# Optimization experiments

Hardware: AMD Instinct MI355X
Metric: run time of the kernel (lower is better)

Reference implementation:

```python
import jax, jax.numpy as jnp
import numpy as np

B, S, D, H = 8, 1024, 512, 8
HD = D // H
NEG = -1000000000.0
LN_EPS = 1e-5


def setup_inputs() -> dict:
    key = jax.random.key(0)
    ks = jax.random.split(key, 16)
    sc = 0.02
    inp = {
        "query": jax.random.normal(ks[0], (B, S, D), jnp.float32),
        "inputs": jax.random.normal(ks[1], (B, S, D), jnp.float32),
        "ren_mat": jax.random.uniform(ks[2], (B, S, S), jnp.float32) * 5.0,
        "timestamp": jax.random.normal(ks[3], (B, S, S), jnp.float32),
        # causal mask: True where attention is disallowed (strictly upper triangular)
        "mask": jnp.triu(jnp.ones((1, S, S), jnp.bool_), k=1),
        "Wq": jax.random.normal(ks[4], (D, D), jnp.float32) * sc,
        "bq": jnp.zeros((D,), jnp.float32),
        "Wk": jax.random.normal(ks[5], (D, D), jnp.float32) * sc,
        "bk": jnp.zeros((D,), jnp.float32),
        "Wv": jax.random.normal(ks[6], (D, D), jnp.float32) * sc,
        "bv": jnp.zeros((D,), jnp.float32),
        "Wo": jax.random.normal(ks[7], (D, D), jnp.float32) * sc,
        "bo": jnp.zeros((D,), jnp.float32),
        "W1": jax.random.normal(ks[8], (D, D), jnp.float32) * sc,
        "b1": jnp.zeros((D,), jnp.float32),
        "ln_g": jnp.ones((D,), jnp.float32),
        "ln_b": jnp.zeros((D,), jnp.float32),
        "l1": jax.random.uniform(ks[9], (1,), jnp.float32),
    }
    return inp


def reference(query, inputs, ren_mat, timestamp, mask,
              Wq, bq, Wk, bk, Wv, bv, Wo, bo, W1, b1, ln_g, ln_b, l1):
    # QKV projections (qk_same=False path; q,k,v all computed from `inputs`)
    def proj(x, W, b):
        return (x @ W.T + b).reshape(B, S, H, HD).transpose(0, 2, 1, 3)  # (B,H,S,HD)

    q = proj(inputs, Wq, bq)
    k = proj(inputs, Wk, bk)
    v = proj(inputs, Wv, bv)

    m = mask[:, None]  # (1,1,S,S), broadcasts over batch & heads

    scores = jnp.einsum("bhqd,bhkd->bhqk", q, k) / jnp.sqrt(jnp.float32(HD))
    scores = jnp.where(m, NEG, scores)
    prob_attn = jax.nn.softmax(scores, axis=-1)

    # memory blend: log10(ren+1) and exp(-|t|), each masked, summed, softmaxed
    ren_feat = jnp.where(m, NEG, jnp.log10(ren_mat + 1.0)[:, None])      # (B,H,S,S)
    time_stamp = jnp.where(m, NEG, jnp.exp(-jnp.abs(timestamp))[:, None])
    mem_attn = jax.nn.softmax(ren_feat + time_stamp, axis=-1)

    l = l1  # (1,) learned blend coefficient
    prob_attn = (1.0 - l) * prob_attn + l * mem_attn

    out = jnp.einsum("bhqk,bhkd->bhqd", prob_attn, v)
    out = out.transpose(0, 2, 1, 3).reshape(B, S, D)
    out = out @ Wo.T + bo

    # residual FFN + layernorm (dropout disabled / eval mode)
    out = out + (out @ W1.T + b1)
    mu = jnp.mean(out, axis=-1, keepdims=True)
    var = jnp.var(out, axis=-1, keepdims=True)
    out = (out - mu) / jnp.sqrt(var + LN_EPS) * ln_g + ln_b
    return out
```

## Files before the change

kernel.cpp:

```cpp
#include <hip/hip_runtime.h>
#include <math.h>

constexpr int kB = 8, kS = 1024, kD = 512, kH = 8, kHD = 64;
constexpr int kM = kB * kS;

typedef __attribute__((ext_vector_type(8))) short s8v;
typedef __attribute__((ext_vector_type(4))) float f4v;
typedef __attribute__((ext_vector_type(4))) unsigned short u4v;

__device__ __forceinline__ unsigned short f2bf(float f) {
    union { float f; unsigned int u; } c; c.f = f;
    unsigned int u = c.u + 0x7FFFu + ((c.u >> 16) & 1u);
    return (unsigned short)(u >> 16);
}

__device__ __forceinline__ void gl2lds(const unsigned short* g, unsigned short* l) {
    __builtin_amdgcn_global_load_lds(
        (const __attribute__((address_space(1))) unsigned int*)g,
        (__attribute__((address_space(3))) unsigned int*)l, 16, 0, 0);
}

__global__ __launch_bounds__(256) void prep_kernel(
    const float* __restrict__ X, const float* __restrict__ Wq,
    const float* __restrict__ Wk, const float* __restrict__ Wv,
    const float* __restrict__ Wo, const float* __restrict__ W1,
    const float* __restrict__ ren, const float* __restrict__ ts,
    const float* __restrict__ bo_g,
    unsigned short* __restrict__ Xbf, unsigned short* __restrict__ Wqkv,
    unsigned short* __restrict__ WoT, unsigned short* __restrict__ W1bf,
    unsigned short* __restrict__ mem)
{
    __shared__ float red[4];
    const int t = threadIdx.x;
    if (blockIdx.x < 5120) {
        const int idx = blockIdx.x * 256 + t;
        const float* src; unsigned short* dst; int off; bool isw1 = false;
        if (idx < 1048576)      { src = X;  dst = Xbf;           off = idx; }
        else if (idx < 1114112) { src = Wq; dst = Wqkv;          off = idx - 1048576; }
        else if (idx < 1179648) { src = Wk; dst = Wqkv + 262144; off = idx - 1114112; }
        else if (idx < 1245184) { src = Wv; dst = Wqkv + 524288; off = idx - 1179648; }
        else                    { src = W1; dst = W1bf;          off = idx - 1245184; isw1 = true; }
        float4 v = ((const float4*)src)[off];
        if (isw1) {
            const int e0 = off * 4;
            const int row = e0 >> 9, col0 = e0 & 511;
            if (row >= col0 && row < col0 + 4) ((float*)&v)[row - col0] += 1.0f;
        }
        u4v p;
        p[0] = f2bf(v.x); p[1] = f2bf(v.y); p[2] = f2bf(v.z); p[3] = f2bf(v.w);
        ((u4v*)dst)[off] = p;
        return;
    }
    if (blockIdx.x >= 13312) {
        const int bi2 = blockIdx.x - 13312;
        if (bi2 < 64) {
            __shared__ float T[64][65];
            const int tr = bi2 >> 3, tc = bi2 & 7;
            const int rr0 = t >> 4, cc0 = (t & 15) * 4;
#pragma unroll
            for (int i2 = 0; i2 < 4; ++i2) {
                const int r = i2 * 16 + rr0;
                const float4 v = *(const float4*)&Wo[(size_t)(tr * 64 + r) * 512 + tc * 64 + cc0];
                T[r][cc0] = v.x; T[r][cc0 + 1] = v.y; T[r][cc0 + 2] = v.z; T[r][cc0 + 3] = v.w;
            }
            __syncthreads();
#pragma unroll
            for (int i2 = 0; i2 < 4; ++i2) {
                const int r2 = i2 * 16 + rr0;
                u4v p;
                p[0] = f2bf(T[cc0][r2]);     p[1] = f2bf(T[cc0 + 1][r2]);
                p[2] = f2bf(T[cc0 + 2][r2]); p[3] = f2bf(T[cc0 + 3][r2]);
                *(u4v*)&WoT[(size_t)(tc * 64 + r2) * 512 + tr * 64 + cc0] = p;
            }
        } else {
            WoT[262144 + t]       = f2bf(bo_g[t]);
            WoT[262144 + 256 + t] = f2bf(bo_g[t + 256]);
        }
        return;
    }
    const int bi = blockIdx.x - 5120;
    const int i = bi & (kS - 1);
    const float* renr = ren + (size_t)bi * kS;
    const float* tsr  = ts  + (size_t)bi * kS;
    unsigned short* memr = mem + (size_t)bi * kS;
    const int j0 = t * 4;
    const float4 r4 = *(const float4*)(renr + j0);
    const float4 t4 = *(const float4*)(tsr + j0);
    float rv[4] = {r4.x, r4.y, r4.z, r4.w};
    float tv[4] = {t4.x, t4.y, t4.z, t4.w};
    float p4[4];
    float lsum = 0.0f;
#pragma unroll
    for (int e = 0; e < 4; ++e) {
        const int j = j0 + e;
        float p = 0.0f;
        if (j <= i) {
            const float val = 0.30102999566f * __log2f(rv[e] + 1.0f) + __expf(-fabsf(tv[e]));
            p = __expf(val);
        }
        p4[e] = p;
        lsum += p;
    }
#pragma unroll
    for (int d = 1; d < 64; d <<= 1) lsum += __shfl_xor(lsum, d);
    if ((t & 63) == 0) red[t >> 6] = lsum;
    __syncthreads();
    const float Z = red[0] + red[1] + red[2] + red[3];
    const float inv = 1.0f / Z;
    u4v pk;
#pragma unroll
    for (int e = 0; e < 4; ++e) pk[e] = f2bf(p4[e] * inv);
    *(u4v*)(memr + j0) = pk;
}

template <int NT>
__device__ __forceinline__ void mfma_core2(
    const unsigned short* __restrict__ A, const unsigned short* __restrict__ B,
    int M0, int N0, unsigned short* As, unsigned short* Bs, f4v (&acc)[4][NT])
{
    const int t = threadIdx.x, w = t >> 6, lane = t & 63;
    const int l16 = lane & 15, quad = lane >> 4;
    const int wm = (w & 1) * 64, wn = (w >> 1) * (NT * 16);
    constexpr int NB = NT / 2;

    const unsigned short* gA[2]; unsigned short* lA[2];
#pragma unroll
    for (int i = 0; i < 2; ++i) {
        const int r0 = w * 32 + i * 16;
        const int r = r0 + (lane >> 2);
        const int c = (lane & 3) ^ ((r >> 1) & 3);
        gA[i] = A + (size_t)(M0 + r) * 512 + c * 8;
        lA[i] = As + r0 * 32;
    }
    const unsigned short* gB[NB]; unsigned short* lB[NB];
#pragma unroll
    for (int i = 0; i < NB; ++i) {
        const int r0 = w * (16 * NB) + i * 16;
        const int r = r0 + (lane >> 2);
        const int c = (lane & 3) ^ ((r >> 1) & 3);
        gB[i] = B + (size_t)(N0 + r) * 512 + c * 8;
        lB[i] = Bs + r0 * 32;
    }

    const f4v zero = {0.0f, 0.0f, 0.0f, 0.0f};
#pragma unroll
    for (int mt = 0; mt < 4; ++mt)
#pragma unroll
        for (int nt = 0; nt < NT; ++nt) acc[mt][nt] = zero;

#pragma unroll 1
    for (int k0 = 0; k0 < 512; k0 += 32) {
        gl2lds(gA[0] + k0, lA[0]);
        gl2lds(gA[1] + k0, lA[1]);
#pragma unroll
        for (int i = 0; i < NB; ++i) gl2lds(gB[i] + k0, lB[i]);
        __syncthreads();
        s8v af[4], bf_[NT];
#pragma unroll
        for (int mt = 0; mt < 4; ++mt) {
            const int r = wm + mt * 16 + l16;
            const int p = r * 4 + (quad ^ ((r >> 1) & 3));
            af[mt] = *(const s8v*)&As[p * 8];
        }
#pragma unroll
        for (int nt = 0; nt < NT; ++nt) {
            const int r = wn + nt * 16 + l16;
            const int p = r * 4 + (quad ^ ((r >> 1) & 3));
            bf_[nt] = *(const s8v*)&Bs[p * 8];
        }
#pragma unroll
        for (int mt = 0; mt < 4; ++mt)
#pragma unroll
            for (int nt = 0; nt < NT; ++nt)
                acc[mt][nt] = __builtin_amdgcn_mfma_f32_16x16x32_bf16(
                    af[mt], bf_[nt], acc[mt][nt], 0, 0, 0);
        __syncthreads();
    }
}

__global__ __launch_bounds__(256) void qkv_mfma_kernel(
    const unsigned short* __restrict__ Xbf, const unsigned short* __restrict__ Wqkv,
    const float* __restrict__ bq, const float* __restrict__ bk, const float* __restrict__ bv,
    const unsigned short* __restrict__ W1bf, const unsigned short* __restrict__ WoT,
    const float* __restrict__ b1,
    unsigned short* __restrict__ qbf, unsigned short* __restrict__ kbf,
    unsigned short* __restrict__ vTbf,
    unsigned short* __restrict__ Wcomb, float* __restrict__ bcomb)
{
    __shared__ __align__(16) unsigned short As[128 * 32];
    __shared__ __align__(16) unsigned short Bs[128 * 32];
    const int y = blockIdx.y;
    const int t = threadIdx.x, w = t >> 6, lane = t & 63;
    const int l16 = lane & 15, quad = lane >> 4;

    if (y == 12) {
        if (blockIdx.x >= 36) return;
        f4v acc[4][2];
        const int M0 = (blockIdx.x / 9) * 128, N0 = (blockIdx.x % 9) * 64;
        mfma_core2<2>(W1bf, WoT, M0, N0, As, Bs, acc);
        const int wm = (w & 1) * 64, wn = (w >> 1) * 32;
#pragma unroll
        for (int nt = 0; nt < 2; ++nt) {
            const int qq = N0 + wn + nt * 16 + l16;
#pragma unroll
            for (int mt = 0; mt < 4; ++mt)
#pragma unroll
                for (int rr = 0; rr < 4; ++rr) {
                    const int m = M0 + wm + mt * 16 + quad * 4 + rr;
                    if (qq < 512)       Wcomb[(size_t)m * 512 + qq] = f2bf(acc[mt][nt][rr]);
                    else if (qq == 512) bcomb[m] = acc[mt][nt][rr] + b1[m];
                }
        }
        return;
    }

    f4v acc[4][4];
    const int wm = (w & 1) * 64, wn = (w >> 1) * 64;
    if (y < 8) {
        const int M0 = blockIdx.x * 128, N0 = y * 128;
        mfma_core2<4>(Xbf, Wqkv, M0, N0, As, Bs, acc);
        const int z = N0 >> 9;
        const float* bias = (z == 0) ? bq : bk;
        unsigned short* out = (z == 0) ? qbf : kbf;
#pragma unroll
        for (int nt = 0; nt < 4; ++nt) {
            const int n512 = (N0 + wn + nt * 16 + l16) & 511;
            const int h = n512 >> 6, hd = n512 & 63;
            const float bv_ = bias[n512];
#pragma unroll
            for (int mt = 0; mt < 4; ++mt) {
#pragma unroll
                for (int rr = 0; rr < 4; ++rr) {
                    const int m = M0 + wm + mt * 16 + quad * 4 + rr;
                    const int b = m >> 10, s = m & (kS - 1);
                    out[(((size_t)b * kH + h) * kS + s) * kHD + hd] =
                        f2bf(acc[mt][nt][rr] + bv_);
                }
            }
        }
    } else {
        const int M0 = (y - 8) * 128, N0 = blockIdx.x * 128;
        mfma_core2<4>(Wqkv + (size_t)1024 * 512, Xbf, M0, N0, As, Bs, acc);
#pragma unroll
        for (int mt = 0; mt < 4; ++mt) {
#pragma unroll
            for (int rr = 0; rr < 4; ++rr) {
                const int vcol = M0 + wm + mt * 16 + quad * 4 + rr;
                const int h = vcol >> 6, hd = vcol & 63;
                const float bv_ = bv[vcol];
#pragma unroll
                for (int nt = 0; nt < 4; ++nt) {
                    const int sg = N0 + wn + nt * 16 + l16;
                    const int b = sg >> 10, s = sg & (kS - 1);
                    vTbf[(((size_t)b * kH + h) * kHD + hd) * kS + s] =
                        f2bf(acc[mt][nt][rr] + bv_);
                }
            }
        }
    }
}

__global__ __launch_bounds__(256) void gemm_final_kernel(
    const unsigned short* __restrict__ Abf, const unsigned short* __restrict__ Wcomb,
    const float* __restrict__ bcomb, float* __restrict__ out)
{
    __shared__ __align__(16) unsigned short As[128 * 32];
    __shared__ __align__(16) unsigned short Bs[64 * 32];
    f4v acc[4][2];
    const int M0 = blockIdx.x * 128, N0 = blockIdx.y * 64;
    mfma_core2<2>(Abf, Wcomb, M0, N0, As, Bs, acc);
    const int t = threadIdx.x, w = t >> 6, lane = t & 63;
    const int l16 = lane & 15, quad = lane >> 4;
    const int wm = (w & 1) * 64, wn = (w >> 1) * 32;
#pragma unroll
    for (int nt = 0; nt < 2; ++nt) {
        const int n = N0 + wn + nt * 16 + l16;
        const float bv_ = bcomb[n];
#pragma unroll
        for (int mt = 0; mt < 4; ++mt)
#pragma unroll
            for (int rr = 0; rr < 4; ++rr) {
                const int m = M0 + wm + mt * 16 + quad * 4 + rr;
                out[(size_t)m * kD + n] = acc[mt][nt][rr] + bv_;
            }
    }
}

#define LDSFRAG(tile, r, c) (*(const s8v*)&(tile)[(size_t)(r) * 64 + ((((c) ^ ((r) & 7))) << 3)])

__global__ __launch_bounds__(256, 4) void flash_attn_kernel(
    const unsigned short* __restrict__ q, const unsigned short* __restrict__ k,
    const unsigned short* __restrict__ vT, const unsigned short* __restrict__ mem,
    const float* __restrict__ l1, unsigned short* __restrict__ aout)
{
    const int qt = 15 - blockIdx.x;
    const int h = blockIdx.y, b = blockIdx.z;
    const int bh = b * kH + h;
    const int t = threadIdx.x;
    const int w = t >> 6, lane = t & 63;
    const int quad = lane >> 4, l16 = lane & 15;
    const float lam = l1[0];

    __shared__ __align__(16) unsigned short KV[2][2][64 * 64];
    __shared__ __align__(16) unsigned short P_lds[4][16 * 64];

    const int qbase = qt * 64;
    const unsigned short* qrow = q + ((size_t)bh * kS + qbase + w * 16 + l16) * kHD;
    const s8v qa0 = *(const s8v*)(qrow + quad * 8);
    const s8v qa1 = *(const s8v*)(qrow + 32 + quad * 8);
    const unsigned short* mbase = mem + ((size_t)b * kS + qbase + w * 16 + l16) * kS;

    const unsigned short* kb = k + (size_t)bh * kS * kHD;
    const unsigned short* vb = vT + (size_t)bh * kHD * kS;

    const unsigned short* gsrc[4];
    int gstep[4];
    unsigned short* ldst[4];
#pragma unroll
    for (int u = 0; u < 4; ++u) {
        const int sp = w * 4 + u;
        const int rloc = (sp & 7) * 8 + (lane >> 3);
        const int chunk = (lane & 7) ^ ((lane >> 3) & 7);
        if (sp < 8) { gsrc[u] = kb + (size_t)rloc * kHD + chunk * 8; gstep[u] = kHD; ldst[u] = &KV[0][0][(sp & 7) * 512]; }
        else        { gsrc[u] = vb + (size_t)rloc * kS  + chunk * 8; gstep[u] = 1;   ldst[u] = &KV[0][1][(sp & 7) * 512]; }
    }

#pragma unroll
    for (int u = 0; u < 4; ++u) gl2lds(gsrc[u], ldst[u]);

    const f4v zero = {0.0f, 0.0f, 0.0f, 0.0f};
    f4v Oa[4], Om[4];
    float lr[4];
#pragma unroll
    for (int nt = 0; nt < 4; ++nt) { Oa[nt] = zero; Om[nt] = zero; lr[nt] = 0.0f; }

    for (int kt = 0; kt <= qt; ++kt) {
        __syncthreads();
        const int cur = kt & 1;
        if (kt < qt) {
            const int jn = (kt + 1) * 64;
            const int boff = ((kt + 1) & 1) * 8192;
#pragma unroll
            for (int u = 0; u < 4; ++u)
                gl2lds(gsrc[u] + (size_t)jn * gstep[u], ldst[u] + boff);
        }
        const int jm = kt * 64;
        const s8v ma0 = *(const s8v*)(mbase + jm + quad * 8);
        const s8v ma1 = *(const s8v*)(mbase + jm + 32 + quad * 8);
        const unsigned short* Kc = &KV[cur][0][0];
        const unsigned short* Vc = &KV[cur][1][0];
        const bool diag = (kt == qt);

#pragma unroll
        for (int ct = 0; ct < 4; ++ct) {
            const int r = ct * 16 + l16;
            const s8v kb0 = LDSFRAG(Kc, r, quad);
            const s8v kb1 = LDSFRAG(Kc, r, 4 + quad);
            f4v acc = zero;
            acc = __builtin_amdgcn_mfma_f32_16x16x32_bf16(qa0, kb0, acc, 0, 0, 0);
            acc = __builtin_amdgcn_mfma_f32_16x16x32_bf16(qa1, kb1, acc, 0, 0, 0);
#pragma unroll
            for (int rr = 0; rr < 4; ++rr) {
                float p = __expf(acc[rr] * 0.125f);
                if (diag && r > (w * 16 + quad * 4 + rr)) p = 0.0f;
                lr[rr] += p;
                const int pr = quad * 4 + rr;
                P_lds[w][pr * 64 + ((((ct * 2 + (l16 >> 3)) ^ (pr & 7)) << 3) | (l16 & 7))] = f2bf(p);
            }
        }
        const s8v pa0 = LDSFRAG(&P_lds[w][0], l16, quad);
        const s8v pa1 = LDSFRAG(&P_lds[w][0], l16, 4 + quad);
#pragma unroll
        for (int nt = 0; nt < 4; ++nt) {
            const int r = nt * 16 + l16;
            const s8v vf0 = LDSFRAG(Vc, r, quad);
            const s8v vf1 = LDSFRAG(Vc, r, 4 + quad);
            Oa[nt] = __builtin_amdgcn_mfma_f32_16x16x32_bf16(pa0, vf0, Oa[nt], 0, 0, 0);
            Oa[nt] = __builtin_amdgcn_mfma_f32_16x16x32_bf16(pa1, vf1, Oa[nt], 0, 0, 0);
            Om[nt] = __builtin_amdgcn_mfma_f32_16x16x32_bf16(ma0, vf0, Om[nt], 0, 0, 0);
            Om[nt] = __builtin_amdgcn_mfma_f32_16x16x32_bf16(ma1, vf1, Om[nt], 0, 0, 0);
        }
    }

    float inv4[4];
#pragma unroll
    for (int rr = 0; rr < 4; ++rr) {
        float Z = lr[rr];
        Z += __shfl_xor(Z, 1);
        Z += __shfl_xor(Z, 2);
        Z += __shfl_xor(Z, 4);
        Z += __shfl_xor(Z, 8);
        inv4[rr] = (1.0f - lam) / Z;
    }
    const int r0 = qbase + w * 16;
#pragma unroll
    for (int nt = 0; nt < 4; ++nt)
#pragma unroll
        for (int rr = 0; rr < 4; ++rr) {
            const int i = r0 + quad * 4 + rr;
            const int d = h * kHD + nt * 16 + l16;
            aout[((size_t)b * kS + i) * kD + d] =
                f2bf(Oa[nt][rr] * inv4[rr] + lam * Om[nt][rr]);
        }
}

__global__ __launch_bounds__(256) void ln_kernel(
    const float* __restrict__ x, const float* __restrict__ g,
    const float* __restrict__ bb, float* __restrict__ out)
{
    const int row = blockIdx.x;
    const int t = threadIdx.x;
    const float* xr = x + (size_t)row * kD;
    float a = xr[t], c = xr[t + 256];
    __shared__ float red[256];
    float s1 = a + c, s2 = a * a + c * c;
    red[t] = s1;
    __syncthreads();
    for (int s = 128; s > 0; s >>= 1) {
        if (t < s) red[t] += red[t + s];
        __syncthreads();
    }
    const float sum = red[0];
    __syncthreads();
    red[t] = s2;
    __syncthreads();
    for (int s = 128; s > 0; s >>= 1) {
        if (t < s) red[t] += red[t + s];
        __syncthreads();
    }
    const float sq = red[0];
    float mu = sum * (1.0f / kD);
    float var = sq * (1.0f / kD) - mu * mu;
    float inv = rsqrtf(var + 1e-5f);
    out[(size_t)row * kD + t]       = (a - mu) * inv * g[t] + bb[t];
    out[(size_t)row * kD + t + 256] = (c - mu) * inv * g[t + 256] + bb[t + 256];
}

extern "C" void kernel_launch(void* const* d_in, const int* in_sizes, int n_in,
                              void* d_out, int out_size, void* d_ws, size_t ws_size,
                              hipStream_t stream) {
    const float* X   = (const float*)d_in[1];
    const float* ren = (const float*)d_in[2];
    const float* ts  = (const float*)d_in[3];
    const float* Wq = (const float*)d_in[5];  const float* bq = (const float*)d_in[6];
    const float* Wk = (const float*)d_in[7];  const float* bk = (const float*)d_in[8];
    const float* Wv = (const float*)d_in[9];  const float* bv = (const float*)d_in[10];
    const float* Wo = (const float*)d_in[11]; const float* bo = (const float*)d_in[12];
    const float* W1 = (const float*)d_in[13]; const float* b1 = (const float*)d_in[14];
    const float* lng = (const float*)d_in[15]; const float* lnb = (const float*)d_in[16];
    const float* l1 = (const float*)d_in[17];
    float* out = (float*)d_out;

    char* wsb = (char*)d_ws;
    unsigned short* Xbf    = (unsigned short*)(wsb);
    unsigned short* Wqkvbf = (unsigned short*)(wsb + (8u  << 20));
    unsigned short* WoTbf  = (unsigned short*)(wsb + (10u << 20));
    unsigned short* W1bf   = (unsigned short*)(wsb + (11u << 20));
    unsigned short* qbf    = (unsigned short*)(wsb + (12u << 20));
    unsigned short* kbf    = (unsigned short*)(wsb + (20u << 20));
    unsigned short* vTbf   = (unsigned short*)(wsb + (28u << 20));
    unsigned short* membf  = (unsigned short*)(wsb + (36u << 20));
    unsigned short* aoutbf = (unsigned short*)(wsb + (52u << 20));
    unsigned short* Wcombf = (unsigned short*)(wsb + (60u << 20));
    float*          bcombf = (float*)        (wsb + (61u << 20));

    prep_kernel<<<dim3(13377), 256, 0, stream>>>(
        X, Wq, Wk, Wv, Wo, W1, ren, ts, bo, Xbf, Wqkvbf, WoTbf, W1bf, membf);
    qkv_mfma_kernel<<<dim3(kM / 128, 13), 256, 0, stream>>>(
        Xbf, Wqkvbf, bq, bk, bv, W1bf, WoTbf, b1, qbf, kbf, vTbf, Wcombf, bcombf);
    flash_attn_kernel<<<dim3(16, kH, kB), 256, 0, stream>>>(
        qbf, kbf, vTbf, membf, l1, aoutbf);
    gemm_final_kernel<<<dim3(kM / 128, kD / 64), 256, 0, stream>>>(
        aoutbf, Wcombf, bcombf, out);
    ln_kernel<<<dim3(kM), 256, 0, stream>>>(out, lng, lnb, out);
}
```

Baseline: 263.1 us.

## Double-buffer GEMM LDS tiles and widen attention key tiles to 128

The shared GEMM core now keeps two LDS buffers, prefetches the next K-slice while computing the current one, and drops one barrier per iteration. The attention kernel processes 128 keys per iteration instead of 64, which halves the loop trip count and barrier count but doubles LDS use, so occupancy is lowered to 2 blocks per CU. The grid is also reordered so batch-head is the fastest-varying dimension. Risks include a partial 128-key tile at the causal edge, which is handled by the mask, and lower occupancy in attention.

```diff
diff --git a/kernel.cpp b/kernel.cpp
--- a/kernel.cpp
+++ b/kernel.cpp
@@ -122,6 +122,8 @@
     const int l16 = lane & 15, quad = lane >> 4;
     const int wm = (w & 1) * 64, wn = (w >> 1) * (NT * 16);
     constexpr int NB = NT / 2;
+    constexpr int ABUF = 128 * 32;
+    constexpr int BBUF = NT * 32 * 32;
 
     const unsigned short* gA[2]; unsigned short* lA[2];
 #pragma unroll
@@ -148,25 +150,34 @@
 #pragma unroll
         for (int nt = 0; nt < NT; ++nt) acc[mt][nt] = zero;
 
+    gl2lds(gA[0], lA[0]);
+    gl2lds(gA[1], lA[1]);
+#pragma unroll
+    for (int i = 0; i < NB; ++i) gl2lds(gB[i], lB[i]);
+
 #pragma unroll 1
     for (int k0 = 0; k0 < 512; k0 += 32) {
-        gl2lds(gA[0] + k0, lA[0]);
-        gl2lds(gA[1] + k0, lA[1]);
-#pragma unroll
-        for (int i = 0; i < NB; ++i) gl2lds(gB[i] + k0, lB[i]);
+        const int cur = (k0 >> 5) & 1;
         __syncthreads();
+        if (k0 + 32 < 512) {
+            const int nb = cur ^ 1;
+            gl2lds(gA[0] + k0 + 32, lA[0] + nb * ABUF);
+            gl2lds(gA[1] + k0 + 32, lA[1] + nb * ABUF);
+#pragma unroll
+            for (int i = 0; i < NB; ++i) gl2lds(gB[i] + k0 + 32, lB[i] + nb * BBUF);
+        }
         s8v af[4], bf_[NT];
 #pragma unroll
         for (int mt = 0; mt < 4; ++mt) {
             const int r = wm + mt * 16 + l16;
             const int p = r * 4 + (quad ^ ((r >> 1) & 3));
-            af[mt] = *(const s8v*)&As[p * 8];
+            af[mt] = *(const s8v*)&As[cur * ABUF + p * 8];
         }
 #pragma unroll
         for (int nt = 0; nt < NT; ++nt) {
             const int r = wn + nt * 16 + l16;
             const int p = r * 4 + (quad ^ ((r >> 1) & 3));
-            bf_[nt] = *(const s8v*)&Bs[p * 8];
+            bf_[nt] = *(const s8v*)&Bs[cur * BBUF + p * 8];
         }
 #pragma unroll
         for (int mt = 0; mt < 4; ++mt)
@@ -174,7 +185,6 @@
             for (int nt = 0; nt < NT; ++nt)
                 acc[mt][nt] = __builtin_amdgcn_mfma_f32_16x16x32_bf16(
                     af[mt], bf_[nt], acc[mt][nt], 0, 0, 0);
-        __syncthreads();
     }
 }
 
@@ -187,8 +197,8 @@
     unsigned short* __restrict__ vTbf,
     unsigned short* __restrict__ Wcomb, float* __restrict__ bcomb)
 {
-    __shared__ __align__(16) unsigned short As[128 * 32];
-    __shared__ __align__(16) unsigned short Bs[128 * 32];
+    __shared__ __align__(16) unsigned short As[2 * 128 * 32];
+    __shared__ __align__(16) unsigned short Bs[2 * 128 * 32];
     const int y = blockIdx.y;
     const int t = threadIdx.x, w = t >> 6, lane = t & 63;
     const int l16 = lane & 15, quad = lane >> 4;
@@ -264,8 +274,8 @@
     const unsigned short* __restrict__ Abf, const unsigned short* __restrict__ Wcomb,
     const float* __restrict__ bcomb, float* __restrict__ out)
 {
-    __shared__ __align__(16) unsigned short As[128 * 32];
-    __shared__ __align__(16) unsigned short Bs[64 * 32];
+    __shared__ __align__(16) unsigned short As[2 * 128 * 32];
+    __shared__ __align__(16) unsigned short Bs[2 * 64 * 32];
     f4v acc[4][2];
     const int M0 = blockIdx.x * 128, N0 = blockIdx.y * 64;
     mfma_core2<2>(Abf, Wcomb, M0, N0, As, Bs, acc);
@@ -286,23 +296,24 @@
     }
 }
 
-#define LDSFRAG(tile, r, c) (*(const s8v*)&(tile)[(size_t)(r) * 64 + ((((c) ^ ((r) & 7))) << 3)])
-
-__global__ __launch_bounds__(256, 4) void flash_attn_kernel(
+#define KFRAG(tile, r, c) (*(const s8v*)&(tile)[(size_t)(r) * 64 + ((((c) ^ ((r) & 7))) << 3)])
+#define VFRAG(tile, r, c) (*(const s8v*)&(tile)[(size_t)(r) * 128 + ((((c) ^ ((r) & 15))) << 3)])
+
+__global__ __launch_bounds__(256, 2) void flash_attn_kernel(
     const unsigned short* __restrict__ q, const unsigned short* __restrict__ k,
     const unsigned short* __restrict__ vT, const unsigned short* __restrict__ mem,
     const float* __restrict__ l1, unsigned short* __restrict__ aout)
 {
-    const int qt = 15 - blockIdx.x;
-    const int h = blockIdx.y, b = blockIdx.z;
-    const int bh = b * kH + h;
+    const int bh = blockIdx.x;
+    const int qt = 15 - blockIdx.y;
+    const int b = bh >> 3, h = bh & 7;
     const int t = threadIdx.x;
     const int w = t >> 6, lane = t & 63;
     const int quad = lane >> 4, l16 = lane & 15;
     const float lam = l1[0];
 
-    __shared__ __align__(16) unsigned short KV[2][2][64 * 64];
-    __shared__ __align__(16) unsigned short P_lds[4][16 * 64];
+    __shared__ __align__(16) unsigned short KV[2][2][64 * 128];
+    __shared__ __align__(16) unsigned short P_lds[4][16 * 128];
 
     const int qbase = qt * 64;
     const unsigned short* qrow = q + ((size_t)bh * kS + qbase + w * 16 + l16) * kHD;
@@ -313,20 +324,33 @@
     const unsigned short* kb = k + (size_t)bh * kS * kHD;
     const unsigned short* vb = vT + (size_t)bh * kHD * kS;
 
-    const unsigned short* gsrc[4];
-    int gstep[4];
-    unsigned short* ldst[4];
-#pragma unroll
-    for (int u = 0; u < 4; ++u) {
-        const int sp = w * 4 + u;
-        const int rloc = (sp & 7) * 8 + (lane >> 3);
-        const int chunk = (lane & 7) ^ ((lane >> 3) & 7);
-        if (sp < 8) { gsrc[u] = kb + (size_t)rloc * kHD + chunk * 8; gstep[u] = kHD; ldst[u] = &KV[0][0][(sp & 7) * 512]; }
-        else        { gsrc[u] = vb + (size_t)rloc * kS  + chunk * 8; gstep[u] = 1;   ldst[u] = &KV[0][1][(sp & 7) * 512]; }
-    }
-
-#pragma unroll
-    for (int u = 0; u < 4; ++u) gl2lds(gsrc[u], ldst[u]);
+    const int nkt = (qt >> 1) + 1;
+
+    const unsigned short* gsrc[8];
+    int gstep[8];
+    unsigned short* ldst[8];
+#pragma unroll
+    for (int u = 0; u < 8; ++u) {
+        const int seg = w * 8 + u;
+        if (seg < 16) {
+            const int s = seg;
+            const int rloc = s * 8 + (lane >> 3);
+            const int chunk = (lane & 7) ^ ((lane >> 3) & 7);
+            gsrc[u] = kb + (size_t)rloc * kHD + chunk * 8;
+            gstep[u] = 128 * kHD;
+            ldst[u] = &KV[0][0][s * 512];
+        } else {
+            const int s = seg - 16;
+            const int d = s * 4 + (lane >> 4);
+            const int chunk = (lane & 15) ^ ((lane >> 4) & 3) ^ ((s & 3) << 2);
+            gsrc[u] = vb + (size_t)d * kS + chunk * 8;
+            gstep[u] = 128;
+            ldst[u] = &KV[0][1][s * 512];
+        }
+    }
+
+#pragma unroll
+    for (int u = 0; u < 8; ++u) gl2lds(gsrc[u], ldst[u]);
 
     const f4v zero = {0.0f, 0.0f, 0.0f, 0.0f};
     f4v Oa[4], Om[4];
@@ -334,51 +358,54 @@
 #pragma unroll
     for (int nt = 0; nt < 4; ++nt) { Oa[nt] = zero; Om[nt] = zero; lr[nt] = 0.0f; }
 
-    for (int kt = 0; kt <= qt; ++kt) {
+    for (int kt = 0; kt < nkt; ++kt) {
         __syncthreads();
         const int cur = kt & 1;
-        if (kt < qt) {
-            const int jn = (kt + 1) * 64;
-            const int boff = ((kt + 1) & 1) * 8192;
-#pragma unroll
-            for (int u = 0; u < 4; ++u)
-                gl2lds(gsrc[u] + (size_t)jn * gstep[u], ldst[u] + boff);
-        }
-        const int jm = kt * 64;
-        const s8v ma0 = *(const s8v*)(mbase + jm + quad * 8);
-        const s8v ma1 = *(const s8v*)(mbase + jm + 32 + quad * 8);
+        if (kt + 1 < nkt) {
+            const int boff = ((kt + 1) & 1) * 16384;
+#pragma unroll
+            for (int u = 0; u < 8; ++u)
+                gl2lds(gsrc[u] + (size_t)(kt + 1) * gstep[u], ldst[u] + boff);
+        }
+        s8v ma[4];
+#pragma unroll
+        for (int ks = 0; ks < 4; ++ks)
+            ma[ks] = *(const s8v*)(mbase + kt * 128 + ks * 32 + quad * 8);
+
         const unsigned short* Kc = &KV[cur][0][0];
         const unsigned short* Vc = &KV[cur][1][0];
-        const bool diag = (kt == qt);
-
-#pragma unroll
-        for (int ct = 0; ct < 4; ++ct) {
+        const bool last = (kt == nkt - 1);
+
+#pragma unroll
+        for (int ct = 0; ct < 8; ++ct) {
             const int r = ct * 16 + l16;
-            const s8v kb0 = LDSFRAG(Kc, r, quad);
-            const s8v kb1 = LDSFRAG(Kc, r, 4 + quad);
+            const s8v kb0 = KFRAG(Kc, r, quad);
+            const s8v kb1 = KFRAG(Kc, r, 4 + quad);
             f4v acc = zero;
             acc = __builtin_amdgcn_mfma_f32_16x16x32_bf16(qa0, kb0, acc, 0, 0, 0);
             acc = __builtin_amdgcn_mfma_f32_16x16x32_bf16(qa1, kb1, acc, 0, 0, 0);
 #pragma unroll
             for (int rr = 0; rr < 4; ++rr) {
                 float p = __expf(acc[rr] * 0.125f);
-                if (diag && r > (w * 16 + quad * 4 + rr)) p = 0.0f;
+                if (last && (kt * 128 + r) > (qbase + w * 16 + quad * 4 + rr)) p = 0.0f;
                 lr[rr] += p;
                 const int pr = quad * 4 + rr;
-                P_lds[w][pr * 64 + ((((ct * 2 + (l16 >> 3)) ^ (pr & 7)) << 3) | (l16 & 7))] = f2bf(p);
-            }
-        }
-        const s8v pa0 = LDSFRAG(&P_lds[w][0], l16, quad);
-        const s8v pa1 = LDSFRAG(&P_lds[w][0], l16, 4 + quad);
+                const int ck = ct * 2 + (l16 >> 3);
+                P_lds[w][pr * 128 + (((ck ^ pr) & 15) << 3) + (l16 & 7)] = f2bf(p);
+            }
+        }
+        s8v pa[4];
+#pragma unroll
+        for (int ks = 0; ks < 4; ++ks)
+            pa[ks] = *(const s8v*)&P_lds[w][l16 * 128 + ((((ks * 4 + quad) ^ l16) & 15) << 3)];
 #pragma unroll
         for (int nt = 0; nt < 4; ++nt) {
-            const int r = nt * 16 + l16;
-            const s8v vf0 = LDSFRAG(Vc, r, quad);
-            const s8v vf1 = LDSFRAG(Vc, r, 4 + quad);
-            Oa[nt] = __builtin_amdgcn_mfma_f32_16x16x32_bf16(pa0, vf0, Oa[nt], 0, 0, 0);
-            Oa[nt] = __builtin_amdgcn_mfma_f32_16x16x32_bf16(pa1, vf1, Oa[nt], 0, 0, 0);
-            Om[nt] = __builtin_amdgcn_mfma_f32_16x16x32_bf16(ma0, vf0, Om[nt], 0, 0, 0);
-            Om[nt] = __builtin_amdgcn_mfma_f32_16x16x32_bf16(ma1, vf1, Om[nt], 0, 0, 0);
+#pragma unroll
+            for (int ks = 0; ks < 4; ++ks) {
+                const s8v vfk = VFRAG(Vc, nt * 16 + l16, ks * 4 + quad);
+                Oa[nt] = __builtin_amdgcn_mfma_f32_16x16x32_bf16(pa[ks], vfk, Oa[nt], 0, 0, 0);
+                Om[nt] = __builtin_amdgcn_mfma_f32_16x16x32_bf16(ma[ks], vfk, Om[nt], 0, 0, 0);
+            }
         }
     }
 
@@ -468,7 +495,7 @@
         X, Wq, Wk, Wv, Wo, W1, ren, ts, bo, Xbf, Wqkvbf, WoTbf, W1bf, membf);
     qkv_mfma_kernel<<<dim3(kM / 128, 13), 256, 0, stream>>>(
         Xbf, Wqkvbf, bq, bk, bv, W1bf, WoTbf, b1, qbf, kbf, vTbf, Wcombf, bcombf);
-    flash_attn_kernel<<<dim3(16, kH, kB), 256, 0, stream>>>(
+    flash_attn_kernel<<<dim3(64, 16), 256, 0, stream>>>(
         qbf, kbf, vTbf, membf, l1, aoutbf);
     gemm_final_kernel<<<dim3(kM / 128, kD / 64), 256, 0, stream>>>(
         aoutbf, Wcombf, bcombf, out);
```

Measured after the change: 249.1 us. 1.06x faster.
